# Optimization experiments

Hardware: AMD Instinct MI355X
Metric: run time of the kernel (lower is better)

Reference implementation:

```python
import jax, jax.numpy as jnp
import numpy as np

BATCH, SEQ, DMODEL, DSTATE = 4, 2048, 1024, 16


def _hippo_legs(N):
    # HiPPO-LegS: A[n,k] = -sqrt(2n+1)sqrt(2k+1) for n>k, -(n+1) on diag; B[n]=sqrt(2n+1)
    n = np.arange(N)
    b = np.sqrt(2.0 * n + 1.0)
    A = -np.tril(np.outer(b, b), -1) - np.diag(n + 1.0)
    return A.astype(np.float32), b.astype(np.float32)


def setup_inputs() -> dict:
    key = jax.random.key(0)
    x = jax.random.normal(key, (BATCH, SEQ, DMODEL), dtype=jnp.float32)
    A_c, B_c = _hippo_legs(DSTATE)
    dt = 1.0 / float(SEQ)  # simple Euler discretization of the continuous HiPPO ODE
    A = jnp.eye(DSTATE, dtype=jnp.float32) + dt * jnp.asarray(A_c)
    Bvec = dt * jnp.asarray(B_c)
    return {"x": x, "A": A, "Bvec": Bvec}


def reference(x, A, Bvec):
    # x: (B, L, D); A: (N, N) discrete transition; Bvec: (N,) input map.
    # Selective-scan recurrence per channel: h_t = A h_{t-1} + Bvec * x_t, y_t = <Bvec, h_t>
    B, L, D = x.shape
    N = Bvec.shape[0]

    def step(h, xt):
        # h: (B, D, N), xt: (B, D)
        h = jnp.einsum('mn,bdn->bdm', A, h) + xt[..., None] * Bvec
        y = h @ Bvec  # (B, D)
        return h, y

    h0 = jnp.zeros((B, D, N), dtype=x.dtype)
    _, ys = jax.lax.scan(step, h0, jnp.moveaxis(x, 1, 0))  # ys: (L, B, D)
    return jnp.moveaxis(ys, 0, 1)  # (B, L, D)
```

## Files before the change

kernel.cpp:

```cpp
#include <hip/hip_runtime.h>

#define BATCH  4
#define SEQL   2048
#define DMODEL 1024
#define NST    16
#define CT     64
#define NCH    (SEQL / CT)

#define WS_P     0
#define WS_W     1024
#define WS_KV    2048
#define WS_APOW  2176
#define WS_HIN   4096

__global__ __launch_bounds__(256) void setup_tables(const float* __restrict__ A,
                                                    const float* __restrict__ Bv,
                                                    float* __restrict__ ws) {
    __shared__ double buf0[256], buf1[256], buf2[256], buf3[256];
    __shared__ double bd[16], vtmp[16];
    double* S  = buf0;
    double* R  = buf1;
    double* Ta = buf2;
    double* Tb = buf3;
    const int t  = threadIdx.x;
    const int i  = t >> 4;
    const int kk = t & 15;
    const int delta = blockIdx.x;

    S[t] = (double)A[t];
    R[t] = (i == kk) ? 1.0 : 0.0;
    if (t < 16) bd[t] = (double)Bv[t];
    __syncthreads();

    for (int sb = 0; sb < 7; ++sb) {
        if ((delta >> sb) & 1) {
            double acc = 0.0;
            #pragma unroll
            for (int l = 0; l < 16; ++l) acc += R[i * 16 + l] * S[l * 16 + kk];
            Ta[t] = acc;
            __syncthreads();
            double* tmp = R; R = Ta; Ta = tmp;
        }
        if (sb < 6) {
            double acc = 0.0;
            #pragma unroll
            for (int l = 0; l < 16; ++l) acc += S[i * 16 + l] * S[l * 16 + kk];
            Tb[t] = acc;
            __syncthreads();
            double* tmp = S; S = Tb; Tb = tmp;
        }
    }

    if (delta < CT) {
        if (t < 16) {
            double acc = 0.0;
            #pragma unroll
            for (int k = 0; k < 16; ++k) acc += R[t * 16 + k] * bd[k];
            ws[WS_P + (CT - 1 - delta) * 16 + t] = (float)acc;
            vtmp[t] = acc;
        }
        __syncthreads();
        if (t == 0) {
            double kd = 0.0;
            for (int m = 0; m < 16; ++m) kd += bd[m] * vtmp[m];
            ws[WS_KV + 63 + delta] = (float)kd;
        }
    }
    if (delta >= 1 && t < 16) {
        double acc = 0.0;
        #pragma unroll
        for (int n = 0; n < 16; ++n) acc += bd[n] * R[n * 16 + t];
        ws[WS_W + (delta - 1) * 16 + t] = (float)acc;
    }
    if (delta == CT) ws[WS_APOW + t] = (float)R[t];
    if (delta == 0 && t < 63) ws[WS_KV + t] = 0.0f;
}

__global__ __launch_bounds__(256) void k1_chunkstate(const float* __restrict__ x,
                                                     const float* __restrict__ ws,
                                                     float* __restrict__ cbuf) {
    __shared__ __align__(16) float xs[CT * 256];
    __shared__ float Ps[CT * 16];
    const int blk = blockIdx.x;
    const int b   = blk >> 7;
    const int j   = (blk >> 2) & 31;
    const int q   = blk & 3;
    const int t   = threadIdx.x;

    const float* __restrict__ xq =
        x + ((size_t)(b * SEQL + j * CT)) * DMODEL + q * 256;

    float4 st[16];
    #pragma unroll
    for (int k = 0; k < 16; ++k) {
        const int f   = k * 256 + t;
        const int row = f >> 6;
        const int c4  = f & 63;
        st[k] = ((const float4*)(xq + (size_t)row * DMODEL))[c4];
    }
    #pragma unroll
    for (int k = 0; k < 4; ++k) Ps[t + k * 256] = ws[WS_P + t + k * 256];
    #pragma unroll
    for (int k = 0; k < 16; ++k) ((float4*)xs)[k * 256 + t] = st[k];
    __syncthreads();

    float c[16];
    #pragma unroll
    for (int m = 0; m < 16; ++m) c[m] = 0.0f;
    #pragma unroll
    for (int s = 0; s < CT; ++s) {
        const float xv = xs[s * 256 + t];
        #pragma unroll
        for (int m = 0; m < 16; ++m)
            c[m] = fmaf(Ps[s * 16 + m], xv, c[m]);
    }

    float4* outp = (float4*)(cbuf + (((size_t)(b * NCH + j) * DMODEL) + q * 256 + t) * 16);
    #pragma unroll
    for (int k = 0; k < 4; ++k)
        outp[k] = make_float4(c[4 * k], c[4 * k + 1], c[4 * k + 2], c[4 * k + 3]);
}

__global__ __launch_bounds__(256) void k2_carry(const float* __restrict__ cbuf,
                                                float* __restrict__ ws) {
    const int blk = blockIdx.x;
    const int b   = blk >> 6;
    const int d0  = (blk & 63) * 16;
    const int t   = threadIdx.x;
    const int m   = t & 15;
    const int ch  = t >> 4;
    const int d   = d0 + ch;
    const int laneBase = t & 48;

    const size_t base0   = (((size_t)(b * NCH) * DMODEL) + d) * 16 + m;
    const size_t jstride = (size_t)DMODEL * 16;

    float cpre[NCH];
    #pragma unroll
    for (int j = 0; j < NCH; ++j)
        cpre[j] = cbuf[base0 + (size_t)j * jstride];

    float Arow[16];
    #pragma unroll
    for (int k = 0; k < 16; ++k) Arow[k] = ws[WS_APOW + m * 16 + k];

    float* hin = ws + WS_HIN;
    float s = 0.0f;
    #pragma unroll
    for (int j = 0; j < NCH; ++j) {
        hin[base0 + (size_t)j * jstride] = s;
        float acc = cpre[j];
        #pragma unroll
        for (int k = 0; k < 16; ++k)
            acc = fmaf(Arow[k], __shfl(s, laneBase + k, 64), acc);
        s = acc;
    }
}

__global__ __launch_bounds__(256) void k3_output(const float* __restrict__ x,
                                                 const float* __restrict__ ws,
                                                 float* __restrict__ y) {
    __shared__ __align__(16) float xs[CT * 256];
    __shared__ float kvs[128];
    __shared__ float Ws[CT * 16];
    const int blk = blockIdx.x;
    const int b   = blk >> 7;
    const int j   = (blk >> 2) & 31;
    const int q   = blk & 3;
    const int t   = threadIdx.x;
    const int d   = q * 256 + t;

    const float* __restrict__ xq =
        x + ((size_t)(b * SEQL + j * CT)) * DMODEL + q * 256;

    float4 st[16];
    #pragma unroll
    for (int k = 0; k < 16; ++k) {
        const int f   = k * 256 + t;
        const int row = f >> 6;
        const int c4  = f & 63;
        st[k] = ((const float4*)(xq + (size_t)row * DMODEL))[c4];
    }
    if (t < 128) kvs[t] = ws[WS_KV + t];
    #pragma unroll
    for (int k = 0; k < 4; ++k) Ws[t + k * 256] = ws[WS_W + t + k * 256];
    const float4* hinp = (const float4*)(ws + WS_HIN +
                         (((size_t)(b * NCH + j) * DMODEL) + d) * 16);
    float4 hv[4];
    #pragma unroll
    for (int k = 0; k < 4; ++k) hv[k] = hinp[k];

    #pragma unroll
    for (int k = 0; k < 16; ++k) ((float4*)xs)[k * 256 + t] = st[k];
    __syncthreads();

    float h[16];
    #pragma unroll
    for (int k = 0; k < 4; ++k) {
        h[4 * k] = hv[k].x; h[4 * k + 1] = hv[k].y;
        h[4 * k + 2] = hv[k].z; h[4 * k + 3] = hv[k].w;
    }

    float* yp = y + ((size_t)(b * SEQL + j * CT)) * DMODEL + d;

    #pragma unroll
    for (int tt = 0; tt < 4; ++tt) {
        float yv[16];
        #pragma unroll
        for (int i = 0; i < 16; ++i) {
            float acc = 0.0f;
            #pragma unroll
            for (int m = 0; m < 16; ++m)
                acc = fmaf(Ws[(tt * 16 + i) * 16 + m], h[m], acc);
            yv[i] = acc;
        }
        #pragma unroll
        for (int s = 0; s < tt * 16 + 16; ++s) {
            const float xv = xs[s * 256 + t];
            #pragma unroll
            for (int i = 0; i < 16; ++i)
                yv[i] = fmaf(kvs[63 + tt * 16 + i - s], xv, yv[i]);
        }
        #pragma unroll
        for (int i = 0; i < 16; ++i)
            yp[(size_t)(tt * 16 + i) * DMODEL] = yv[i];
    }
}

extern "C" void kernel_launch(void* const* d_in, const int* in_sizes, int n_in,
                              void* d_out, int out_size, void* d_ws, size_t ws_size,
                              hipStream_t stream) {
    (void)in_sizes; (void)n_in; (void)out_size; (void)ws_size;
    const float* x  = (const float*)d_in[0];
    const float* A  = (const float*)d_in[1];
    const float* Bv = (const float*)d_in[2];
    float* out = (float*)d_out;
    float* ws  = (float*)d_ws;

    setup_tables<<<65, 256, 0, stream>>>(A, Bv, ws);
    k1_chunkstate<<<512, 256, 0, stream>>>(x, ws, out);
    k2_carry<<<256, 256, 0, stream>>>(out, ws);
    k3_output<<<512, 256, 0, stream>>>(x, ws, out);
}
```

Before: 129.0 us.

## Split x chunk staging into two halves and read coefficient tables directly from global

In both the chunk-state and output kernels, the 64-row x tile is now loaded in two halves. The second half's global loads are issued before the first half's compute, so memory latency overlaps with arithmetic. The P, W and kv coefficient tables are no longer staged in shared memory; they are read directly from global memory with uniform addresses, which the compiler can turn into scalar loads. This removes the shared staging and one sync's worth of setup, but adds a second barrier, and correctness relies on scalar or cached loads of the tables being cheap.

```diff
diff --git a/kernel.cpp b/kernel.cpp
--- a/kernel.cpp
+++ b/kernel.cpp
@@ -80,7 +80,6 @@
                                                      const float* __restrict__ ws,
                                                      float* __restrict__ cbuf) {
     __shared__ __align__(16) float xs[CT * 256];
-    __shared__ float Ps[CT * 16];
     const int blk = blockIdx.x;
     const int b   = blk >> 7;
     const int j   = (blk >> 2) & 31;
@@ -89,30 +88,50 @@
 
     const float* __restrict__ xq =
         x + ((size_t)(b * SEQL + j * CT)) * DMODEL + q * 256;
-
-    float4 st[16];
-    #pragma unroll
-    for (int k = 0; k < 16; ++k) {
+    const float* __restrict__ P = ws + WS_P;
+
+    float4 stA[8];
+    #pragma unroll
+    for (int k = 0; k < 8; ++k) {
         const int f   = k * 256 + t;
         const int row = f >> 6;
         const int c4  = f & 63;
-        st[k] = ((const float4*)(xq + (size_t)row * DMODEL))[c4];
-    }
-    #pragma unroll
-    for (int k = 0; k < 4; ++k) Ps[t + k * 256] = ws[WS_P + t + k * 256];
-    #pragma unroll
-    for (int k = 0; k < 16; ++k) ((float4*)xs)[k * 256 + t] = st[k];
-    __syncthreads();
+        stA[k] = ((const float4*)(xq + (size_t)row * DMODEL))[c4];
+    }
+    #pragma unroll
+    for (int k = 0; k < 8; ++k) ((float4*)xs)[k * 256 + t] = stA[k];
+    __syncthreads();
+
+    float4 stB[8];
+    #pragma unroll
+    for (int k = 0; k < 8; ++k) {
+        const int f   = k * 256 + t;
+        const int row = 32 + (f >> 6);
+        const int c4  = f & 63;
+        stB[k] = ((const float4*)(xq + (size_t)row * DMODEL))[c4];
+    }
 
     float c[16];
     #pragma unroll
     for (int m = 0; m < 16; ++m) c[m] = 0.0f;
     #pragma unroll
-    for (int s = 0; s < CT; ++s) {
+    for (int s = 0; s < 32; ++s) {
         const float xv = xs[s * 256 + t];
         #pragma unroll
         for (int m = 0; m < 16; ++m)
-            c[m] = fmaf(Ps[s * 16 + m], xv, c[m]);
+            c[m] = fmaf(P[s * 16 + m], xv, c[m]);
+    }
+
+    #pragma unroll
+    for (int k = 0; k < 8; ++k) ((float4*)xs)[(8 + k) * 256 + t] = stB[k];
+    __syncthreads();
+
+    #pragma unroll
+    for (int s = 32; s < CT; ++s) {
+        const float xv = xs[s * 256 + t];
+        #pragma unroll
+        for (int m = 0; m < 16; ++m)
+            c[m] = fmaf(P[s * 16 + m], xv, c[m]);
     }
 
     float4* outp = (float4*)(cbuf + (((size_t)(b * NCH + j) * DMODEL) + q * 256 + t) * 16);
@@ -161,8 +180,6 @@
                                                  const float* __restrict__ ws,
                                                  float* __restrict__ y) {
     __shared__ __align__(16) float xs[CT * 256];
-    __shared__ float kvs[128];
-    __shared__ float Ws[CT * 16];
     const int blk = blockIdx.x;
     const int b   = blk >> 7;
     const int j   = (blk >> 2) & 31;
@@ -172,18 +189,17 @@
 
     const float* __restrict__ xq =
         x + ((size_t)(b * SEQL + j * CT)) * DMODEL + q * 256;
-
-    float4 st[16];
-    #pragma unroll
-    for (int k = 0; k < 16; ++k) {
+    const float* __restrict__ Wt = ws + WS_W;
+    const float* __restrict__ kv = ws + WS_KV + 63;
+
+    float4 stA[8];
+    #pragma unroll
+    for (int k = 0; k < 8; ++k) {
         const int f   = k * 256 + t;
         const int row = f >> 6;
         const int c4  = f & 63;
-        st[k] = ((const float4*)(xq + (size_t)row * DMODEL))[c4];
-    }
-    if (t < 128) kvs[t] = ws[WS_KV + t];
-    #pragma unroll
-    for (int k = 0; k < 4; ++k) Ws[t + k * 256] = ws[WS_W + t + k * 256];
+        stA[k] = ((const float4*)(xq + (size_t)row * DMODEL))[c4];
+    }
     const float4* hinp = (const float4*)(ws + WS_HIN +
                          (((size_t)(b * NCH + j) * DMODEL) + d) * 16);
     float4 hv[4];
@@ -191,8 +207,17 @@
     for (int k = 0; k < 4; ++k) hv[k] = hinp[k];
 
     #pragma unroll
-    for (int k = 0; k < 16; ++k) ((float4*)xs)[k * 256 + t] = st[k];
-    __syncthreads();
+    for (int k = 0; k < 8; ++k) ((float4*)xs)[k * 256 + t] = stA[k];
+    __syncthreads();
+
+    float4 stB[8];
+    #pragma unroll
+    for (int k = 0; k < 8; ++k) {
+        const int f   = k * 256 + t;
+        const int row = 32 + (f >> 6);
+        const int c4  = f & 63;
+        stB[k] = ((const float4*)(xq + (size_t)row * DMODEL))[c4];
+    }
 
     float h[16];
     #pragma unroll
@@ -204,14 +229,14 @@
     float* yp = y + ((size_t)(b * SEQL + j * CT)) * DMODEL + d;
 
     #pragma unroll
-    for (int tt = 0; tt < 4; ++tt) {
+    for (int tt = 0; tt < 2; ++tt) {
         float yv[16];
         #pragma unroll
         for (int i = 0; i < 16; ++i) {
             float acc = 0.0f;
             #pragma unroll
             for (int m = 0; m < 16; ++m)
-                acc = fmaf(Ws[(tt * 16 + i) * 16 + m], h[m], acc);
+                acc = fmaf(Wt[(tt * 16 + i) * 16 + m], h[m], acc);
             yv[i] = acc;
         }
         #pragma unroll
@@ -219,7 +244,34 @@
             const float xv = xs[s * 256 + t];
             #pragma unroll
             for (int i = 0; i < 16; ++i)
-                yv[i] = fmaf(kvs[63 + tt * 16 + i - s], xv, yv[i]);
+                yv[i] = fmaf(kv[tt * 16 + i - s], xv, yv[i]);
+        }
+        #pragma unroll
+        for (int i = 0; i < 16; ++i)
+            yp[(size_t)(tt * 16 + i) * DMODEL] = yv[i];
+    }
+
+    #pragma unroll
+    for (int k = 0; k < 8; ++k) ((float4*)xs)[(8 + k) * 256 + t] = stB[k];
+    __syncthreads();
+
+    #pragma unroll
+    for (int tt = 2; tt < 4; ++tt) {
+        float yv[16];
+        #pragma unroll
+        for (int i = 0; i < 16; ++i) {
+            float acc = 0.0f;
+            #pragma unroll
+            for (int m = 0; m < 16; ++m)
+                acc = fmaf(Wt[(tt * 16 + i) * 16 + m], h[m], acc);
+            yv[i] = acc;
+        }
+        #pragma unroll
+        for (int s = 0; s < tt * 16 + 16; ++s) {
+            const float xv = xs[s * 256 + t];
+            #pragma unroll
+            for (int i = 0; i < 16; ++i)
+                yv[i] = fmaf(kv[tt * 16 + i - s], xv, yv[i]);
         }
         #pragma unroll
         for (int i = 0; i < 16; ++i)
```

Result: slower. 140.0 us (+8.5%).
